# Kernel optimization log

Hardware: AMD Instinct MI355X
Metric: run time of the kernel (lower is better)

Reference implementation:

```python
import jax, jax.numpy as jnp
import numpy as np

D_MODEL = 1024
NHEAD = 16
HEAD_DIM = D_MODEL // NHEAD
D_FF = 4096
EPS = 1e-5


def _linear(x, w, b):
    # torch Linear: y = x @ W^T + b, W is [out, in]
    return x @ w.T + b


def _layernorm(x, g, b):
    mu = jnp.mean(x, axis=-1, keepdims=True)
    var = jnp.var(x, axis=-1, keepdims=True)
    return (x - mu) * jax.lax.rsqrt(var + EPS) * g + b


def setup_inputs() -> dict:
    key = jax.random.key(0)
    ks = jax.random.split(key, 16)
    s = 0.02
    inp = {
        'x': jax.random.normal(ks[0], (2048, D_MODEL), jnp.float32),
        'q_in_w': s * jax.random.normal(ks[1], (D_MODEL, D_MODEL), jnp.float32),
        'q_in_b': jnp.zeros((D_MODEL,), jnp.float32),
        'k_in_w': s * jax.random.normal(ks[2], (D_MODEL, D_MODEL), jnp.float32),
        'k_in_b': jnp.zeros((D_MODEL,), jnp.float32),
        'v_in_w': s * jax.random.normal(ks[3], (D_MODEL, D_MODEL), jnp.float32),
        'v_in_b': jnp.zeros((D_MODEL,), jnp.float32),
        'out_w': s * jax.random.normal(ks[4], (D_MODEL, D_MODEL), jnp.float32),
        'out_b': jnp.zeros((D_MODEL,), jnp.float32),
        'ffn1_w': s * jax.random.normal(ks[5], (D_FF, D_MODEL), jnp.float32),
        'ffn1_b': jnp.zeros((D_FF,), jnp.float32),
        'ffn2_w': s * jax.random.normal(ks[6], (D_MODEL, D_FF), jnp.float32),
        'ffn2_b': jnp.zeros((D_MODEL,), jnp.float32),
        'n1_g': jnp.ones((D_MODEL,), jnp.float32),
        'n1_b': jnp.zeros((D_MODEL,), jnp.float32),
        'n2_g': jnp.ones((D_MODEL,), jnp.float32),
        'n2_b': jnp.zeros((D_MODEL,), jnp.float32),
        'q_out_w': s * jax.random.normal(ks[7], (D_MODEL, D_MODEL), jnp.float32),
        'q_out_b': jnp.zeros((D_MODEL,), jnp.float32),
        'k_out_w': s * jax.random.normal(ks[8], (D_MODEL, D_MODEL), jnp.float32),
        'k_out_b': jnp.zeros((D_MODEL,), jnp.float32),
        'v_out_w': s * jax.random.normal(ks[9], (D_MODEL, D_MODEL), jnp.float32),
        'v_out_b': jnp.zeros((D_MODEL,), jnp.float32),
        'seq_length': 2048,
    }
    return inp


def reference(x, q_in_w, q_in_b, k_in_w, k_in_b, v_in_w, v_in_b,
              out_w, out_b, ffn1_w, ffn1_b, ffn2_w, ffn2_b,
              n1_g, n1_b, n2_g, n2_b,
              q_out_w, q_out_b, k_out_w, k_out_b, v_out_w, v_out_b,
              seq_length):
    S = seq_length
    # --- is_first: batched in-projections (replaces per-token loop + cat) ---
    q_buf = _linear(x, q_in_w, q_in_b)   # [S, D]
    k_buf = _linear(x, k_in_w, k_in_b)
    v_buf = _linear(x, v_in_w, v_in_b)
    prev_layer_input = x

    # --- multi-head attention (non-causal, no mask) ---
    q = q_buf.reshape(S, NHEAD, HEAD_DIM).transpose(1, 0, 2)  # [H, S, Dh]
    k = k_buf.reshape(S, NHEAD, HEAD_DIM).transpose(1, 0, 2)
    v = v_buf.reshape(S, NHEAD, HEAD_DIM).transpose(1, 0, 2)
    scale = 1.0 / np.sqrt(HEAD_DIM).astype(np.float32)
    scores = jnp.einsum('hqd,hkd->hqk', q, k) * scale        # [H, S, S]
    attn = jax.nn.softmax(scores, axis=-1)
    ctx = jnp.einsum('hqk,hkd->hqd', attn, v)                # [H, S, Dh]
    attn_output = ctx.transpose(1, 0, 2).reshape(S, D_MODEL)  # [S, D]

    # --- post-norm residual blocks (batched over tokens) ---
    h = _linear(attn_output, out_w, out_b)
    h = _layernorm(prev_layer_input + h, n1_g, n1_b)
    ff = _linear(jax.nn.relu(_linear(h, ffn1_w, ffn1_b)), ffn2_w, ffn2_b)
    y = _layernorm(h + ff, n2_g, n2_b)                        # [S, D]

    # --- not is_last: out-projections for the next layer ---
    q_next = _linear(y, q_out_w, q_out_b)
    k_next = _linear(y, k_out_w, k_out_b)
    v_next = _linear(y, v_out_w, v_out_b)
    return (q_next, k_next, v_next, y)
```

## Files before the change

### kernel.cpp

```cpp
#include <hip/hip_runtime.h>
#include <math.h>

#define SEQ   2048
#define DM    1024
#define NH    16
#define DH    64
#define DFF   4096
#define KVSPLIT 4

typedef __bf16 bf16;
using bf16x8 = __attribute__((ext_vector_type(8))) __bf16;
using f32x4  = __attribute__((ext_vector_type(4))) float;

__device__ __forceinline__ unsigned short f2bfu(float f) {
    unsigned int u = __float_as_uint(f);
    u += 0x7FFF + ((u >> 16) & 1);
    return (unsigned short)(u >> 16);
}
__device__ __forceinline__ bf16 f2bf(float f) {
    unsigned short s = f2bfu(f);
    return __builtin_bit_cast(bf16, s);
}

__device__ __forceinline__ void gll16(const bf16* g, bf16* lds_base) {
    __builtin_amdgcn_global_load_lds(
        (const __attribute__((address_space(1))) unsigned int*)g,
        (__attribute__((address_space(3))) unsigned int*)lds_base, 16, 0, 0);
}

__global__ __launch_bounds__(256) void conv_k(const float* __restrict__ src,
                                              bf16* __restrict__ dst, int n) {
    int i = (blockIdx.x * 256 + threadIdx.x) * 4;
    if (i >= n) return;
    float4 v = *(const float4*)(src + i);
    ushort4 o;
    o.x = f2bfu(v.x); o.y = f2bfu(v.y); o.z = f2bfu(v.z); o.w = f2bfu(v.w);
    *(ushort4*)((unsigned short*)dst + i) = o;
}

struct ConvSeg  { const float* src; bf16* dst; int n; };
struct ConvSegs { ConvSeg s[6]; };

__global__ __launch_bounds__(256) void conv_multi_k(ConvSegs cs) {
    ConvSeg sg = cs.s[blockIdx.y];
    int i = (blockIdx.x * 256 + threadIdx.x) * 4;
    if (i >= sg.n) return;
    float4 v = *(const float4*)(sg.src + i);
    ushort4 o;
    o.x = f2bfu(v.x); o.y = f2bfu(v.y); o.z = f2bfu(v.z); o.w = f2bfu(v.w);
    *(ushort4*)((unsigned short*)sg.dst + i) = o;
}

struct GemmPtrs {
    const bf16* W[3];
    const float* bias[3];
    float* out32[3];
    bf16*  out16[3];
};

template<int BM, int BN>
__global__ __launch_bounds__(256) void gemm_bf16_k(
    const bf16* __restrict__ A, const float* __restrict__ res,
    GemmPtrs p, int N, int K, int relu)
{
    constexpr int TM = BM / 32;
    constexpr int TN = BN / 32;
    __shared__ bf16 As[BM][32];
    __shared__ bf16 Ws[BN][32];

    const int t    = threadIdx.x;
    const int lane = t & 63;
    const int wave = t >> 6;
    const int quad = lane >> 4;
    const int l15  = lane & 15;
    const int wm   = (wave >> 1) * (BM / 2);
    const int wn   = (wave & 1) * (BN / 2);
    const int m0   = blockIdx.y * BM;
    const int n0   = blockIdx.x * BN;
    const bf16* __restrict__ W = p.W[blockIdx.z];

    f32x4 acc[TM][TN];
    #pragma unroll
    for (int i = 0; i < TM; ++i)
        #pragma unroll
        for (int j = 0; j < TN; ++j)
            acc[i][j] = f32x4{0.f, 0.f, 0.f, 0.f};

    for (int k0 = 0; k0 < K; k0 += 32) {
        #pragma unroll
        for (int s = 0; s < BM / 64; ++s) {
            int base = s * 256 + wave * 64;
            int idx  = base + lane;
            gll16(A + (long)(m0 + (idx >> 2)) * K + k0 + (idx & 3) * 8,
                  &As[0][0] + (long)base * 8);
        }
        #pragma unroll
        for (int s = 0; s < BN / 64; ++s) {
            int base = s * 256 + wave * 64;
            int idx  = base + lane;
            gll16(W + (long)(n0 + (idx >> 2)) * K + k0 + (idx & 3) * 8,
                  &Ws[0][0] + (long)base * 8);
        }
        __syncthreads();

        bf16x8 a[TM], b[TN];
        #pragma unroll
        for (int i = 0; i < TM; ++i)
            a[i] = *(const bf16x8*)&As[wm + i * 16 + l15][quad * 8];
        #pragma unroll
        for (int j = 0; j < TN; ++j)
            b[j] = *(const bf16x8*)&Ws[wn + j * 16 + l15][quad * 8];
        #pragma unroll
        for (int i = 0; i < TM; ++i)
            #pragma unroll
            for (int j = 0; j < TN; ++j)
                acc[i][j] = __builtin_amdgcn_mfma_f32_16x16x32_bf16(
                    a[i], b[j], acc[i][j], 0, 0, 0);
        __syncthreads();
    }

    float* o32 = p.out32[blockIdx.z];
    bf16*  o16 = p.out16[blockIdx.z];
    const float* bias = p.bias[blockIdx.z];
    #pragma unroll
    for (int j = 0; j < TN; ++j) {
        int n = n0 + wn + j * 16 + l15;
        float bv = bias[n];
        #pragma unroll
        for (int i = 0; i < TM; ++i) {
            #pragma unroll
            for (int r = 0; r < 4; ++r) {
                int m = m0 + wm + i * 16 + quad * 4 + r;
                float v = acc[i][j][r] + bv;
                if (res)  v += res[(long)m * N + n];
                if (relu) v = fmaxf(v, 0.f);
                if (o32) o32[(long)m * N + n] = v;
                if (o16) o16[(long)m * N + n] = f2bf(v);
            }
        }
    }
}

__global__ __launch_bounds__(256) void attn_mfma_k(
    const bf16* __restrict__ Q, const bf16* __restrict__ Kg,
    const bf16* __restrict__ Vg, bf16* __restrict__ Opart,
    float* __restrict__ lpart)
{
    __shared__ bf16 Kb[64][72];
    __shared__ bf16 Vt[64][72];
    __shared__ bf16 Pw[4][16][76];

    const int t    = threadIdx.x;
    const int lane = t & 63;
    const int wave = t >> 6;
    const int quad = lane >> 4;
    const int l15  = lane & 15;
    const int h    = blockIdx.y;
    const int q0   = blockIdx.x * 64;
    const int spl  = blockIdx.z;
    const int cb   = h * DH;
    const long SD  = (long)SEQ * DM;

    const int qrow = q0 + wave * 16 + l15;
    bf16x8 aQ[2];
    #pragma unroll
    for (int kh = 0; kh < 2; ++kh)
        aQ[kh] = *(const bf16x8*)(Q + (long)qrow * DM + cb + kh * 32 + quad * 8);

    bf16 oneb = f2bf(l15 == 0 ? 1.0f : 0.0f);
    bf16x8 bOnes;
    #pragma unroll
    for (int j = 0; j < 8; ++j) bOnes[j] = oneb;

    f32x4 o_acc[4], l_acc;
    #pragma unroll
    for (int dt = 0; dt < 4; ++dt) o_acc[dt] = f32x4{0.f, 0.f, 0.f, 0.f};
    l_acc = f32x4{0.f, 0.f, 0.f, 0.f};

    const float SCL = 0.18033688f;
    const int kv_lo = spl * (SEQ / KVSPLIT);
    const int kv_hi = kv_lo + SEQ / KVSPLIT;

    for (int kv0 = kv_lo; kv0 < kv_hi; kv0 += 64) {
        __syncthreads();
        #pragma unroll
        for (int s = 0; s < 2; ++s) {
            int idx = t + s * 256;
            int key = idx >> 3;
            int dg  = idx & 7;
            *(uint4*)&Kb[key][dg * 8] =
                *(const uint4*)(Kg + (long)(kv0 + key) * DM + cb + dg * 8);
            bf16x8 vv = *(const bf16x8*)(Vg + (long)(kv0 + key) * DM + cb + dg * 8);
            int swz = key ^ (dg * 8);
            #pragma unroll
            for (int j = 0; j < 8; ++j) Vt[dg * 8 + j][swz] = vv[j];
        }
        __syncthreads();

        f32x4 s4[4];
        #pragma unroll
        for (int kt = 0; kt < 4; ++kt) {
            bf16x8 b0 = *(const bf16x8*)&Kb[kt * 16 + l15][quad * 8];
            bf16x8 b1 = *(const bf16x8*)&Kb[kt * 16 + l15][32 + quad * 8];
            f32x4 s = f32x4{0.f, 0.f, 0.f, 0.f};
            s = __builtin_amdgcn_mfma_f32_16x16x32_bf16(aQ[0], b0, s, 0, 0, 0);
            s = __builtin_amdgcn_mfma_f32_16x16x32_bf16(aQ[1], b1, s, 0, 0, 0);
            s4[kt] = s;
        }

        #pragma unroll
        for (int kt = 0; kt < 4; ++kt) {
            #pragma unroll
            for (int r = 0; r < 4; ++r) {
                float pv = exp2f(s4[kt][r] * SCL);
                unsigned u = __float_as_uint(pv) + 0x8000u;
                Pw[wave][quad * 4 + r][kt * 16 + l15] =
                    __builtin_bit_cast(bf16, (unsigned short)(u >> 16));
            }
        }
        bf16x8 aP[2];
        aP[0] = *(const bf16x8*)&Pw[wave][l15][quad * 8];
        aP[1] = *(const bf16x8*)&Pw[wave][l15][32 + quad * 8];

        l_acc = __builtin_amdgcn_mfma_f32_16x16x32_bf16(aP[0], bOnes, l_acc, 0, 0, 0);
        l_acc = __builtin_amdgcn_mfma_f32_16x16x32_bf16(aP[1], bOnes, l_acc, 0, 0, 0);

        #pragma unroll
        for (int dt = 0; dt < 4; ++dt) {
            int d   = dt * 16 + l15;
            int dgr = d >> 3;
            bf16x8 v0 = *(const bf16x8*)&Vt[d][((quad) ^ dgr) * 8];
            bf16x8 v1 = *(const bf16x8*)&Vt[d][((4 + quad) ^ dgr) * 8];
            o_acc[dt] = __builtin_amdgcn_mfma_f32_16x16x32_bf16(aP[0], v0, o_acc[dt], 0, 0, 0);
            o_acc[dt] = __builtin_amdgcn_mfma_f32_16x16x32_bf16(aP[1], v1, o_acc[dt], 0, 0, 0);
        }
    }

    #pragma unroll
    for (int r = 0; r < 4; ++r) {
        int row = q0 + wave * 16 + quad * 4 + r;
        #pragma unroll
        for (int dt = 0; dt < 4; ++dt)
            Opart[(long)spl * SD + (long)row * DM + cb + dt * 16 + l15] =
                f2bf(o_acc[dt][r]);
        if (l15 == 0)
            lpart[((long)spl * NH + h) * SEQ + row] = l_acc[r];
    }
}

__global__ __launch_bounds__(256) void attn_reduce_k(
    const bf16* __restrict__ Opart, const float* __restrict__ lpart,
    bf16* __restrict__ O)
{
    const long SD = (long)SEQ * DM;
    long i = ((long)blockIdx.x * 256 + threadIdx.x) * 8;
    int row = (int)(i / DM);
    int h   = (int)((i % DM) / DH);

    float l = 0.f;
    #pragma unroll
    for (int k = 0; k < KVSPLIT; ++k)
        l += lpart[((long)k * NH + h) * SEQ + row];
    float inv = 1.f / l;

    float acc[8] = {};
    #pragma unroll
    for (int k = 0; k < KVSPLIT; ++k) {
        bf16x8 v = *(const bf16x8*)(Opart + (long)k * SD + i);
        #pragma unroll
        for (int j = 0; j < 8; ++j) acc[j] += (float)v[j];
    }
    bf16x8 o;
    #pragma unroll
    for (int j = 0; j < 8; ++j) o[j] = f2bf(acc[j] * inv);
    *(bf16x8*)(O + i) = o;
}

__global__ __launch_bounds__(256) void ln_k(
    const float* __restrict__ X, const float* __restrict__ g,
    const float* __restrict__ b, float* __restrict__ out,
    bf16* __restrict__ out16)
{
    const int row = blockIdx.x;
    const int t   = threadIdx.x;
    const float* xr = X + (long)row * DM;

    float4 v = *(const float4*)(xr + (t << 2));
    float s1 = v.x + v.y + v.z + v.w;
    float s2 = v.x * v.x + v.y * v.y + v.z * v.z + v.w * v.w;
    #pragma unroll
    for (int off = 32; off > 0; off >>= 1) {
        s1 += __shfl_xor(s1, off);
        s2 += __shfl_xor(s2, off);
    }
    __shared__ float red[8];
    int wid = t >> 6, lid = t & 63;
    if (lid == 0) { red[wid] = s1; red[4 + wid] = s2; }
    __syncthreads();
    s1 = red[0] + red[1] + red[2] + red[3];
    s2 = red[4] + red[5] + red[6] + red[7];

    float mu   = s1 * (1.f / DM);
    float var  = s2 * (1.f / DM) - mu * mu;
    float rstd = rsqrtf(var + 1e-5f);

    float4 gv = *(const float4*)(g + (t << 2));
    float4 bv = *(const float4*)(b + (t << 2));
    float4 ov;
    ov.x = (v.x - mu) * rstd * gv.x + bv.x;
    ov.y = (v.y - mu) * rstd * gv.y + bv.y;
    ov.z = (v.z - mu) * rstd * gv.z + bv.z;
    ov.w = (v.w - mu) * rstd * gv.w + bv.w;
    *(float4*)(out + (long)row * DM + (t << 2)) = ov;
    if (out16) {
        ushort4 o;
        o.x = f2bfu(ov.x); o.y = f2bfu(ov.y); o.z = f2bfu(ov.z); o.w = f2bfu(ov.w);
        *(ushort4*)((unsigned short*)out16 + (long)row * DM + (t << 2)) = o;
    }
}

extern "C" void kernel_launch(void* const* d_in, const int* in_sizes, int n_in,
                              void* d_out, int out_size, void* d_ws, size_t ws_size,
                              hipStream_t stream)
{
    const float* x       = (const float*)d_in[0];
    const float* q_in_w  = (const float*)d_in[1];
    const float* q_in_b  = (const float*)d_in[2];
    const float* k_in_w  = (const float*)d_in[3];
    const float* k_in_b  = (const float*)d_in[4];
    const float* v_in_w  = (const float*)d_in[5];
    const float* v_in_b  = (const float*)d_in[6];
    const float* out_w   = (const float*)d_in[7];
    const float* out_b   = (const float*)d_in[8];
    const float* ffn1_w  = (const float*)d_in[9];
    const float* ffn1_b  = (const float*)d_in[10];
    const float* ffn2_w  = (const float*)d_in[11];
    const float* ffn2_b  = (const float*)d_in[12];
    const float* n1_g    = (const float*)d_in[13];
    const float* n1_b    = (const float*)d_in[14];
    const float* n2_g    = (const float*)d_in[15];
    const float* n2_b    = (const float*)d_in[16];
    const float* q_out_w = (const float*)d_in[17];
    const float* q_out_b = (const float*)d_in[18];
    const float* k_out_w = (const float*)d_in[19];
    const float* k_out_b = (const float*)d_in[20];
    const float* v_out_w = (const float*)d_in[21];
    const float* v_out_b = (const float*)d_in[22];

    float* out = (float*)d_out;
    const long SD = (long)SEQ * DM;
    const long MB = 1024 * 1024;

    char* w = (char*)d_ws;
    bf16* xbf    = (bf16*)(w);
    bf16* qb     = (bf16*)(w + 4  * MB);
    bf16* kb     = (bf16*)(w + 8  * MB);
    bf16* vb     = (bf16*)(w + 12 * MB);
    bf16* atnb   = (bf16*)(w + 16 * MB);
    bf16* f1     = (bf16*)(w + 4  * MB);
    bf16* Opart  = (bf16*)(w + 20 * MB);
    float* lpart = (float*)(w + 36 * MB);
    float* tmp   = (float*)(w + 20 * MB);
    bf16* h16    = (bf16*)(w + 28 * MB);
    bf16* wqi    = (bf16*)(w + 32 * MB);
    bf16* wki    = (bf16*)(w + 34 * MB);
    bf16* wvi    = (bf16*)(w + 36 * MB);
    bf16* wo     = (bf16*)(w + 38 * MB);
    bf16* wf2    = (bf16*)(w + 32 * MB);
    bf16* wf1    = (bf16*)(w + 40 * MB);
    bf16* wqo    = (bf16*)(w + 40 * MB);
    bf16* wko    = (bf16*)(w + 42 * MB);
    bf16* wvo    = (bf16*)(w + 44 * MB);
    bf16* ybf    = (bf16*)(w);
    float* y32   = out + 3 * SD;

    dim3 blk(256);
    const int DD = DM * DM;

    {
        ConvSegs cs;
        cs.s[0] = {x,      xbf, (int)SD};
        cs.s[1] = {q_in_w, wqi, DD};
        cs.s[2] = {k_in_w, wki, DD};
        cs.s[3] = {v_in_w, wvi, DD};
        cs.s[4] = {out_w,  wo,  DD};
        cs.s[5] = {ffn1_w, wf1, DM * DFF};
        conv_multi_k<<<dim3(DM * DFF / 1024, 6), blk, 0, stream>>>(cs);
    }

    {
        GemmPtrs p{};
        p.W[0] = wqi; p.W[1] = wki; p.W[2] = wvi;
        p.bias[0] = q_in_b; p.bias[1] = k_in_b; p.bias[2] = v_in_b;
        p.out16[0] = qb; p.out16[1] = kb; p.out16[2] = vb;
        gemm_bf16_k<128, 64><<<dim3(DM / 64, SEQ / 128, 3), blk, 0, stream>>>(
            xbf, nullptr, p, DM, DM, 0);
    }

    attn_mfma_k<<<dim3(SEQ / 64, NH, KVSPLIT), blk, 0, stream>>>(
        qb, kb, vb, Opart, lpart);
    attn_reduce_k<<<dim3((int)(SD / 2048)), blk, 0, stream>>>(Opart, lpart, atnb);

    {
        GemmPtrs p{};
        p.W[0] = wo; p.bias[0] = out_b; p.out32[0] = tmp;
        gemm_bf16_k<64, 64><<<dim3(DM / 64, SEQ / 64, 1), blk, 0, stream>>>(
            atnb, x, p, DM, DM, 0);
    }
    conv_k<<<dim3(DM * DFF / 1024), blk, 0, stream>>>(ffn2_w, wf2, DM * DFF);

    ln_k<<<SEQ, blk, 0, stream>>>(tmp, n1_g, n1_b, tmp, h16);

    {
        GemmPtrs p{};
        p.W[0] = wf1; p.bias[0] = ffn1_b; p.out16[0] = f1;
        gemm_bf16_k<128, 64><<<dim3(DFF / 64, SEQ / 128, 1), blk, 0, stream>>>(
            h16, nullptr, p, DFF, DM, 1);
    }
    {
        ConvSegs cs;
        cs.s[0] = {q_out_w, wqo, DD};
        cs.s[1] = {k_out_w, wko, DD};
        cs.s[2] = {v_out_w, wvo, DD};
        cs.s[3] = cs.s[0]; cs.s[4] = cs.s[0]; cs.s[5] = cs.s[0];
        conv_multi_k<<<dim3(DD / 1024, 3), blk, 0, stream>>>(cs);
    }

    {
        GemmPtrs p{};
        p.W[0] = wf2; p.bias[0] = ffn2_b; p.out32[0] = y32;
        gemm_bf16_k<64, 64><<<dim3(DM / 64, SEQ / 64, 1), blk, 0, stream>>>(
            f1, tmp, p, DM, DFF, 0);
    }
    ln_k<<<SEQ, blk, 0, stream>>>(y32, n2_g, n2_b, y32, ybf);

    {
        GemmPtrs p{};
        p.W[0] = wqo; p.W[1] = wko; p.W[2] = wvo;
        p.bias[0] = q_out_b; p.bias[1] = k_out_b; p.bias[2] = v_out_b;
        p.out32[0] = out; p.out32[1] = out + SD; p.out32[2] = out + 2 * SD;
        gemm_bf16_k<128, 64><<<dim3(DM / 64, SEQ / 128, 3), blk, 0, stream>>>(
            ybf, nullptr, p, DM, DM, 0);
    }
}
```

Before: 370.8 us.

## Split-K the out-projection and FFN2 GEMMs and fuse reduction into LayerNorm

```diff
diff --git a/kernel.cpp b/kernel.cpp
--- a/kernel.cpp
+++ b/kernel.cpp
@@ -60,8 +60,7 @@
 
 template<int BM, int BN>
 __global__ __launch_bounds__(256) void gemm_bf16_k(
-    const bf16* __restrict__ A, const float* __restrict__ res,
-    GemmPtrs p, int N, int K, int relu)
+    const bf16* __restrict__ A, GemmPtrs p, int N, int K, int relu)
 {
     constexpr int TM = BM / 32;
     constexpr int TN = BN / 32;
@@ -132,12 +131,88 @@
             for (int r = 0; r < 4; ++r) {
                 int m = m0 + wm + i * 16 + quad * 4 + r;
                 float v = acc[i][j][r] + bv;
-                if (res)  v += res[(long)m * N + n];
                 if (relu) v = fmaxf(v, 0.f);
                 if (o32) o32[(long)m * N + n] = v;
                 if (o16) o16[(long)m * N + n] = f2bf(v);
             }
         }
+    }
+}
+
+template<int BM, int BN, int KS>
+__global__ __launch_bounds__(256) void gemm_splitk_k(
+    const bf16* __restrict__ A, const bf16* __restrict__ W,
+    float* __restrict__ part, int N, int K)
+{
+    constexpr int TM = BM / 32;
+    constexpr int TN = BN / 32;
+    __shared__ bf16 As[BM][32];
+    __shared__ bf16 Ws[BN][32];
+
+    const int t    = threadIdx.x;
+    const int lane = t & 63;
+    const int wave = t >> 6;
+    const int quad = lane >> 4;
+    const int l15  = lane & 15;
+    const int wm   = (wave >> 1) * (BM / 2);
+    const int wn   = (wave & 1) * (BN / 2);
+    const int m0   = blockIdx.y * BM;
+    const int n0   = blockIdx.x * BN;
+    const int Kp   = K / KS;
+    const int klo  = blockIdx.z * Kp;
+    const long MN  = (long)gridDim.y * BM * N;
+
+    f32x4 acc[TM][TN];
+    #pragma unroll
+    for (int i = 0; i < TM; ++i)
+        #pragma unroll
+        for (int j = 0; j < TN; ++j)
+            acc[i][j] = f32x4{0.f, 0.f, 0.f, 0.f};
+
+    for (int k0 = klo; k0 < klo + Kp; k0 += 32) {
+        #pragma unroll
+        for (int s = 0; s < BM / 64; ++s) {
+            int base = s * 256 + wave * 64;
+            int idx  = base + lane;
+            gll16(A + (long)(m0 + (idx >> 2)) * K + k0 + (idx & 3) * 8,
+                  &As[0][0] + (long)base * 8);
+        }
+        #pragma unroll
+        for (int s = 0; s < BN / 64; ++s) {
+            int base = s * 256 + wave * 64;
+            int idx  = base + lane;
+            gll16(W + (long)(n0 + (idx >> 2)) * K + k0 + (idx & 3) * 8,
+                  &Ws[0][0] + (long)base * 8);
+        }
+        __syncthreads();
+
+        bf16x8 a[TM], b[TN];
+        #pragma unroll
+        for (int i = 0; i < TM; ++i)
+            a[i] = *(const bf16x8*)&As[wm + i * 16 + l15][quad * 8];
+        #pragma unroll
+        for (int j = 0; j < TN; ++j)
+            b[j] = *(const bf16x8*)&Ws[wn + j * 16 + l15][quad * 8];
+        #pragma unroll
+        for (int i = 0; i < TM; ++i)
+            #pragma unroll
+            for (int j = 0; j < TN; ++j)
+                acc[i][j] = __builtin_amdgcn_mfma_f32_16x16x32_bf16(
+                    a[i], b[j], acc[i][j], 0, 0, 0);
+        __syncthreads();
+    }
+
+    float* o = part + (long)blockIdx.z * MN;
+    #pragma unroll
+    for (int j = 0; j < TN; ++j) {
+        int n = n0 + wn + j * 16 + l15;
+        #pragma unroll
+        for (int i = 0; i < TM; ++i)
+            #pragma unroll
+            for (int r = 0; r < 4; ++r) {
+                int m = m0 + wm + i * 16 + quad * 4 + r;
+                o[(long)m * N + n] = acc[i][j][r];
+            }
     }
 }
 
@@ -276,22 +351,33 @@
     *(bf16x8*)(O + i) = o;
 }
 
-__global__ __launch_bounds__(256) void ln_k(
-    const float* __restrict__ X, const float* __restrict__ g,
-    const float* __restrict__ b, float* __restrict__ out,
+template<int NS>
+__global__ __launch_bounds__(256) void ln_red_k(
+    const float* __restrict__ part, const float* __restrict__ bias,
+    const float* __restrict__ res, const float* __restrict__ g,
+    const float* __restrict__ b, float* __restrict__ out32,
     bf16* __restrict__ out16)
 {
+    const long SD = (long)SEQ * DM;
     const int row = blockIdx.x;
     const int t   = threadIdx.x;
-    const float* xr = X + (long)row * DM;
-
-    float4 v = *(const float4*)(xr + (t << 2));
+    const long off = (long)row * DM + (t << 2);
+
+    float4 v = *(const float4*)(res + off);
+    float4 bv0 = *(const float4*)(bias + (t << 2));
+    v.x += bv0.x; v.y += bv0.y; v.z += bv0.z; v.w += bv0.w;
+    #pragma unroll
+    for (int z = 0; z < NS; ++z) {
+        float4 pz = *(const float4*)(part + z * SD + off);
+        v.x += pz.x; v.y += pz.y; v.z += pz.z; v.w += pz.w;
+    }
+
     float s1 = v.x + v.y + v.z + v.w;
     float s2 = v.x * v.x + v.y * v.y + v.z * v.z + v.w * v.w;
     #pragma unroll
-    for (int off = 32; off > 0; off >>= 1) {
-        s1 += __shfl_xor(s1, off);
-        s2 += __shfl_xor(s2, off);
+    for (int off2 = 32; off2 > 0; off2 >>= 1) {
+        s1 += __shfl_xor(s1, off2);
+        s2 += __shfl_xor(s2, off2);
     }
     __shared__ float red[8];
     int wid = t >> 6, lid = t & 63;
@@ -311,11 +397,11 @@
     ov.y = (v.y - mu) * rstd * gv.y + bv.y;
     ov.z = (v.z - mu) * rstd * gv.z + bv.z;
     ov.w = (v.w - mu) * rstd * gv.w + bv.w;
-    *(float4*)(out + (long)row * DM + (t << 2)) = ov;
+    if (out32) *(float4*)(out32 + off) = ov;
     if (out16) {
         ushort4 o;
         o.x = f2bfu(ov.x); o.y = f2bfu(ov.y); o.z = f2bfu(ov.z); o.w = f2bfu(ov.w);
-        *(ushort4*)((unsigned short*)out16 + (long)row * DM + (t << 2)) = o;
+        *(ushort4*)((unsigned short*)out16 + off) = o;
     }
 }
 
@@ -352,26 +438,28 @@
     const long MB = 1024 * 1024;
 
     char* w = (char*)d_ws;
-    bf16* xbf    = (bf16*)(w);
-    bf16* qb     = (bf16*)(w + 4  * MB);
-    bf16* kb     = (bf16*)(w + 8  * MB);
-    bf16* vb     = (bf16*)(w + 12 * MB);
-    bf16* atnb   = (bf16*)(w + 16 * MB);
-    bf16* f1     = (bf16*)(w + 4  * MB);
-    bf16* Opart  = (bf16*)(w + 20 * MB);
-    float* lpart = (float*)(w + 36 * MB);
-    float* tmp   = (float*)(w + 20 * MB);
-    bf16* h16    = (bf16*)(w + 28 * MB);
-    bf16* wqi    = (bf16*)(w + 32 * MB);
-    bf16* wki    = (bf16*)(w + 34 * MB);
-    bf16* wvi    = (bf16*)(w + 36 * MB);
-    bf16* wo     = (bf16*)(w + 38 * MB);
-    bf16* wf2    = (bf16*)(w + 32 * MB);
-    bf16* wf1    = (bf16*)(w + 40 * MB);
-    bf16* wqo    = (bf16*)(w + 40 * MB);
-    bf16* wko    = (bf16*)(w + 42 * MB);
-    bf16* wvo    = (bf16*)(w + 44 * MB);
-    bf16* ybf    = (bf16*)(w);
+    bf16*  xbf   = (bf16*)(w);
+    float* lpart = (float*)(w);
+    bf16*  qb    = (bf16*)(w + 4  * MB);
+    bf16*  kb    = (bf16*)(w + 8  * MB);
+    bf16*  vb    = (bf16*)(w + 12 * MB);
+    bf16*  atnb  = (bf16*)(w + 16 * MB);
+    float* h32   = (float*)(w);
+    bf16*  h16   = (bf16*)(w + 8  * MB);
+    float* P2    = (float*)(w + 8  * MB);
+    bf16*  Opart = (bf16*)(w + 20 * MB);
+    float* P1    = (float*)(w + 20 * MB);
+    bf16*  f1    = (bf16*)(w + 24 * MB);
+    bf16*  wqi   = (bf16*)(w + 32 * MB);
+    bf16*  wki   = (bf16*)(w + 34 * MB);
+    bf16*  wvi   = (bf16*)(w + 36 * MB);
+    bf16*  wo    = (bf16*)(w + 38 * MB);
+    bf16*  wf1   = (bf16*)(w + 40 * MB);
+    bf16*  wf2   = (bf16*)(w + 40 * MB);
+    bf16*  wqo   = (bf16*)(w + 24 * MB);
+    bf16*  wko   = (bf16*)(w + 26 * MB);
+    bf16*  wvo   = (bf16*)(w + 28 * MB);
+    bf16*  ybf   = (bf16*)(w + 30 * MB);
     float* y32   = out + 3 * SD;
 
     dim3 blk(256);
@@ -394,29 +482,30 @@
         p.bias[0] = q_in_b; p.bias[1] = k_in_b; p.bias[2] = v_in_b;
         p.out16[0] = qb; p.out16[1] = kb; p.out16[2] = vb;
         gemm_bf16_k<128, 64><<<dim3(DM / 64, SEQ / 128, 3), blk, 0, stream>>>(
-            xbf, nullptr, p, DM, DM, 0);
+            xbf, p, DM, DM, 0);
     }
 
     attn_mfma_k<<<dim3(SEQ / 64, NH, KVSPLIT), blk, 0, stream>>>(
         qb, kb, vb, Opart, lpart);
     attn_reduce_k<<<dim3((int)(SD / 2048)), blk, 0, stream>>>(Opart, lpart, atnb);
 
-    {
-        GemmPtrs p{};
-        p.W[0] = wo; p.bias[0] = out_b; p.out32[0] = tmp;
-        gemm_bf16_k<64, 64><<<dim3(DM / 64, SEQ / 64, 1), blk, 0, stream>>>(
-            atnb, x, p, DM, DM, 0);
-    }
-    conv_k<<<dim3(DM * DFF / 1024), blk, 0, stream>>>(ffn2_w, wf2, DM * DFF);
-
-    ln_k<<<SEQ, blk, 0, stream>>>(tmp, n1_g, n1_b, tmp, h16);
+    gemm_splitk_k<64, 128, 2><<<dim3(DM / 128, SEQ / 64, 2), blk, 0, stream>>>(
+        atnb, wo, P1, DM, DM);
+
+    ln_red_k<2><<<SEQ, blk, 0, stream>>>(P1, out_b, x, n1_g, n1_b, h32, h16);
 
     {
         GemmPtrs p{};
         p.W[0] = wf1; p.bias[0] = ffn1_b; p.out16[0] = f1;
         gemm_bf16_k<128, 64><<<dim3(DFF / 64, SEQ / 128, 1), blk, 0, stream>>>(
-            h16, nullptr, p, DFF, DM, 1);
-    }
+            h16, p, DFF, DM, 1);
+    }
+
+    conv_k<<<dim3(DM * DFF / 1024), blk, 0, stream>>>(ffn2_w, wf2, DM * DFF);
+
+    gemm_splitk_k<64, 128, 2><<<dim3(DM / 128, SEQ / 64, 2), blk, 0, stream>>>(
+        f1, wf2, P2, DM, DFF);
+
     {
         ConvSegs cs;
         cs.s[0] = {q_out_w, wqo, DD};
@@ -426,13 +515,7 @@
         conv_multi_k<<<dim3(DD / 1024, 3), blk, 0, stream>>>(cs);
     }
 
-    {
-        GemmPtrs p{};
-        p.W[0] = wf2; p.bias[0] = ffn2_b; p.out32[0] = y32;
-        gemm_bf16_k<64, 64><<<dim3(DM / 64, SEQ / 64, 1), blk, 0, stream>>>(
-            f1, tmp, p, DM, DFF, 0);
-    }
-    ln_k<<<SEQ, blk, 0, stream>>>(y32, n2_g, n2_b, y32, ybf);
+    ln_red_k<2><<<SEQ, blk, 0, stream>>>(P2, ffn2_b, h32, n2_g, n2_b, y32, ybf);
 
     {
         GemmPtrs p{};
@@ -440,6 +523,6 @@
         p.bias[0] = q_out_b; p.bias[1] = k_out_b; p.bias[2] = v_out_b;
         p.out32[0] = out; p.out32[1] = out + SD; p.out32[2] = out + 2 * SD;
         gemm_bf16_k<128, 64><<<dim3(DM / 64, SEQ / 128, 3), blk, 0, stream>>>(
-            ybf, nullptr, p, DM, DM, 0);
-    }
-}
+            ybf, p, DM, DM, 0);
+    }
+}
```

After: 355.6 us. -4.1%, faster.
